# Performance work log

Hardware: AMD Instinct MI355X
Metric: run time of the kernel (lower is better)

Reference implementation:

```python
import jax, jax.numpy as jnp
import numpy as np

HIDDEN = 512
TEXT_DIM = 768
NUM_HEADS = 8
NUM_GROUPS = 32
GN_EPS = 1e-5
COS_EPS = 1e-6


def setup_inputs() -> dict:
    key = jax.random.key(0)
    ks = jax.random.split(key, 9)
    s = 0.02
    return {
        "x": jax.random.normal(ks[0], (16, HIDDEN, 64, 64), jnp.float32),
        "text_emb": jax.random.normal(ks[1], (16, 77, TEXT_DIM), jnp.float32),
        "gn_weight": jnp.ones((HIDDEN,), jnp.float32),
        "gn_bias": jnp.zeros((HIDDEN,), jnp.float32),
        "Wq": jax.random.normal(ks[2], (HIDDEN, HIDDEN), jnp.float32) * s,
        "Wk": jax.random.normal(ks[3], (HIDDEN, TEXT_DIM), jnp.float32) * s,
        "Wv": jax.random.normal(ks[4], (HIDDEN, TEXT_DIM), jnp.float32) * s,
        "Wo": jax.random.normal(ks[5], (HIDDEN, HIDDEN), jnp.float32) * s,
        "bo": jnp.zeros((HIDDEN,), jnp.float32),
    }


def reference(x, text_emb, gn_weight, gn_bias, Wq, Wk, Wv, Wo, bo):
    B, C, H, W = x.shape
    N_img = H * W
    nh, hd = NUM_HEADS, C // NUM_HEADS

    # GroupNorm(32, C): normalize over (channels-in-group, H, W)
    xg = x.reshape(B, NUM_GROUPS, -1)
    mu = xg.mean(axis=-1, keepdims=True)
    var = jnp.mean(jnp.square(xg - mu), axis=-1, keepdims=True)
    xn = ((xg - mu) * jax.lax.rsqrt(var + GN_EPS)).reshape(B, C, H, W)
    xn = xn * gn_weight[None, :, None, None] + gn_bias[None, :, None, None]

    x_flat = xn.reshape(B, C, N_img).transpose(0, 2, 1)  # [B, N_img, C]

    q = jnp.einsum('bnc,dc->bnd', x_flat, Wq)            # [B, N_img, C]
    k = jnp.einsum('btc,dc->btd', text_emb, Wk)          # [B, N_text, C]
    v = jnp.einsum('btc,dc->btd', text_emb, Wv)

    # split heads -> [B, nh, N, hd]
    q = q.reshape(B, N_img, nh, hd).transpose(0, 2, 1, 3)
    k = k.reshape(B, -1, nh, hd).transpose(0, 2, 1, 3)
    v = v.reshape(B, -1, nh, hd).transpose(0, 2, 1, 3)

    # cosine-sim attention: L2-normalize q and k, scale = 1.0
    q = q / (jnp.linalg.norm(q, axis=-1, keepdims=True) + COS_EPS)
    k = k / (jnp.linalg.norm(k, axis=-1, keepdims=True) + COS_EPS)

    scores = jnp.einsum('bhqd,bhkd->bhqk', q, k)         # [B, nh, N_img, N_text]
    attn = jax.nn.softmax(scores, axis=-1)
    out = jnp.einsum('bhqk,bhkd->bhqd', attn, v)         # [B, nh, N_img, hd]

    out = out.transpose(0, 2, 1, 3).reshape(B, N_img, C)
    out = jnp.einsum('bnc,dc->bnd', out, Wo) + bo
    out = out.transpose(0, 2, 1).reshape(B, C, H, W)
    return x + out
```

## Files before the change

### kernel.cpp

```cpp
#include <hip/hip_runtime.h>
#include <math.h>


typedef unsigned short u16;
typedef __attribute__((ext_vector_type(8))) __bf16 bf16x8;
typedef __attribute__((ext_vector_type(4))) float f32x4;

typedef __attribute__((address_space(1))) unsigned int as1_u32;
typedef __attribute__((address_space(3))) unsigned int as3_u32;

__device__ __forceinline__ float b2f(u16 u) {
  union { unsigned int i; float f; } c; c.i = ((unsigned int)u) << 16; return c.f;
}
__device__ __forceinline__ u16 f2b(float f) {
  union { float f; unsigned int i; } c; c.f = f;
  unsigned int i = c.i + 0x7fffu + ((c.i >> 16) & 1u);
  return (u16)(i >> 16);
}

__device__ __forceinline__ void g2lds16(const void* g, void* l) {
  __builtin_amdgcn_global_load_lds((const as1_u32*)g, (as3_u32*)l, 16, 0, 0);
}

__global__ void k_cast(const float* __restrict__ in, u16* __restrict__ out, int n) {
  int i = blockIdx.x * 256 + threadIdx.x;
  int st = gridDim.x * 256;
  for (; i < n; i += st) out[i] = f2b(in[i]);
}

__global__ __launch_bounds__(256) void k_gnstats(const float* __restrict__ x,
                                                 float* __restrict__ stats) {
  int bg = blockIdx.x;
  const float4* p = (const float4*)(x + (size_t)bg * 65536);
  float s = 0.f, ss = 0.f;
  for (int i = threadIdx.x; i < 16384; i += 256) {
    float4 v = p[i];
    s  += v.x + v.y + v.z + v.w;
    ss += v.x*v.x + v.y*v.y + v.z*v.z + v.w*v.w;
  }
  for (int o = 1; o < 64; o <<= 1) { s += __shfl_xor(s, o, 64); ss += __shfl_xor(ss, o, 64); }
  __shared__ float as_[4], bs_[4];
  int w = threadIdx.x >> 6;
  if ((threadIdx.x & 63) == 0) { as_[w] = s; bs_[w] = ss; }
  __syncthreads();
  if (threadIdx.x == 0) {
    s  = as_[0] + as_[1] + as_[2] + as_[3];
    ss = bs_[0] + bs_[1] + bs_[2] + bs_[3];
    float mu  = s * (1.f / 65536.f);
    float var = ss * (1.f / 65536.f) - mu * mu;
    stats[2*bg]   = mu;
    stats[2*bg+1] = rsqrtf(var + 1e-5f);
  }
}

__global__ __launch_bounds__(256) void k_gnapply(
    const float* __restrict__ x, const float* __restrict__ stats,
    const float* __restrict__ gw, const float* __restrict__ gb,
    u16* __restrict__ xn) {
  __shared__ float tile[64][65];
  const int b = blockIdx.z, c0 = blockIdx.y << 6, hw0 = blockIdx.x << 6;
  const int t = threadIdx.x;
  const int tl16 = t & 15;
#pragma unroll
  for (int i = 0; i < 4; ++i) {
    const int cl = (i << 4) + (t >> 4);
    const int c = c0 + cl;
    const int sg = (b << 5) + (c >> 4);
    const float mu = stats[2*sg], rs = stats[2*sg+1];
    const float wgt = gw[c] * rs, bs = gb[c] - mu * wgt;
    const float4 v = *(const float4*)(x + (((size_t)b << 9) + c) * 4096 + hw0 + (tl16 << 2));
    tile[cl][(tl16 << 2) + 0] = v.x * wgt + bs;
    tile[cl][(tl16 << 2) + 1] = v.y * wgt + bs;
    tile[cl][(tl16 << 2) + 2] = v.z * wgt + bs;
    tile[cl][(tl16 << 2) + 3] = v.w * wgt + bs;
  }
  __syncthreads();
#pragma unroll
  for (int i = 0; i < 4; ++i) {
    const int hl = (i << 4) + (t >> 4);
    const int c4 = tl16 << 2;
    ushort4 o;
    o.x = f2b(tile[c4 + 0][hl]);
    o.y = f2b(tile[c4 + 1][hl]);
    o.z = f2b(tile[c4 + 2][hl]);
    o.w = f2b(tile[c4 + 3][hl]);
    *(ushort4*)(xn + ((size_t)((b << 12) + hw0 + hl)) * 512 + c0 + c4) = o;
  }
}

template <int MODE>
__global__ __launch_bounds__(256) void k_gemm(
    const u16* __restrict__ A, const u16* __restrict__ BT,
    int M, int N, int K,
    float* __restrict__ outf, u16* __restrict__ outb,
    const float* __restrict__ xres, const float* __restrict__ bias) {
  __shared__ u16 Al[2][128 * 64];
  __shared__ u16 Bl[2][128 * 64];
  const int tid = threadIdx.x;
  const int l = tid & 63, w = tid >> 6;

  const int nwg = gridDim.x * gridDim.y;
  int lin = blockIdx.y * gridDim.x + blockIdx.x;
  lin = (lin & 7) * (nwg >> 3) + (lin >> 3);
  const int m0 = (lin / gridDim.x) << 7, n0 = (lin % gridDim.x) << 7;

  const int wm = (w >> 1) << 6, wn = (w & 1) << 6;
  const int lr = l & 15, lg = l >> 4;

  f32x4 acc[4][4];
#pragma unroll
  for (int i = 0; i < 4; ++i)
#pragma unroll
    for (int j = 0; j < 4; ++j) acc[i][j] = {0.f, 0.f, 0.f, 0.f};

  const int rl = l >> 3, slot = l & 7;
  const int c8 = (slot ^ rl) << 3;
  int arow[4], brow[4];
#pragma unroll
  for (int j = 0; j < 4; ++j) {
    const int r_local = (w << 5) + (j << 3) + rl;
    arow[j] = min(m0 + r_local, M - 1);
    brow[j] = n0 + r_local;
  }

  const int ksteps = K >> 6;

#pragma unroll
  for (int j = 0; j < 4; ++j)
    g2lds16(A + (size_t)arow[j] * K + c8, Al[0] + (((w << 5) + (j << 3)) << 6));
#pragma unroll
  for (int j = 0; j < 4; ++j)
    g2lds16(BT + (size_t)brow[j] * K + c8, Bl[0] + (((w << 5) + (j << 3)) << 6));
  __syncthreads();

  for (int ks = 0; ks < ksteps; ++ks) {
    const int cur = ks & 1, nxt = cur ^ 1;
    if (ks + 1 < ksteps) {
      const int kb = ((ks + 1) << 6) + c8;
#pragma unroll
      for (int j = 0; j < 4; ++j)
        g2lds16(A + (size_t)arow[j] * K + kb, Al[nxt] + (((w << 5) + (j << 3)) << 6));
#pragma unroll
      for (int j = 0; j < 4; ++j)
        g2lds16(BT + (size_t)brow[j] * K + kb, Bl[nxt] + (((w << 5) + (j << 3)) << 6));
    }
    bf16x8 bfr[4][2];
#pragma unroll
    for (int j = 0; j < 4; ++j) {
      const int br = wn + j * 16 + lr;
      bfr[j][0] = *(const bf16x8*)(Bl[cur] + (br << 6) + (((lg    ) ^ (br & 7)) << 3));
      bfr[j][1] = *(const bf16x8*)(Bl[cur] + (br << 6) + (((lg + 4) ^ (br & 7)) << 3));
    }
#pragma unroll
    for (int i = 0; i < 4; ++i) {
      const int ar = wm + i * 16 + lr;
      const bf16x8 a0 = *(const bf16x8*)(Al[cur] + (ar << 6) + (((lg    ) ^ (ar & 7)) << 3));
      const bf16x8 a1 = *(const bf16x8*)(Al[cur] + (ar << 6) + (((lg + 4) ^ (ar & 7)) << 3));
#pragma unroll
      for (int j = 0; j < 4; ++j) {
        acc[i][j] = __builtin_amdgcn_mfma_f32_16x16x32_bf16(a0, bfr[j][0], acc[i][j], 0, 0, 0);
        acc[i][j] = __builtin_amdgcn_mfma_f32_16x16x32_bf16(a1, bfr[j][1], acc[i][j], 0, 0, 0);
      }
    }
    __syncthreads();
  }

  const int lg4 = lg << 2;
  if (MODE == 3) {
#pragma unroll
    for (int i = 0; i < 4; ++i) {
#pragma unroll
      for (int r = 0; r < 4; ++r) {
        float ss = 0.f;
#pragma unroll
        for (int j = 0; j < 4; ++j) { const float v = acc[i][j][r]; ss += v * v; }
        ss += __shfl_xor(ss, 1, 64); ss += __shfl_xor(ss, 2, 64);
        ss += __shfl_xor(ss, 4, 64); ss += __shfl_xor(ss, 8, 64);
        const float sc = 1.f / (sqrtf(ss) + 1e-6f);
        const int row = m0 + wm + i * 16 + lg4 + r;
#pragma unroll
        for (int j = 0; j < 4; ++j)
          outb[(size_t)row * N + n0 + wn + j * 16 + lr] = f2b(acc[i][j][r] * sc);
      }
    }
    return;
  }
#pragma unroll
  for (int i = 0; i < 4; ++i) {
#pragma unroll
    for (int j = 0; j < 4; ++j) {
#pragma unroll
      for (int r = 0; r < 4; ++r) {
        const int row = m0 + wm + i * 16 + lg4 + r;
        const int col = n0 + wn + j * 16 + lr;
        const float v = acc[i][j][r];
        if (MODE == 0) {
          if (row < M) outf[(size_t)row * N + col] = v;
        } else if (MODE == 1) {
          outb[(size_t)row * N + col] = f2b(v);
        } else {
          const int bb = col >> 12, hw = col & 4095;
          const size_t o = (((size_t)bb << 9) + row) * 4096 + hw;
          outf[o] = xres[o] + bias[row] + v;
        }
      }
    }
  }
}

__global__ __launch_bounds__(64) void k_kvnorm(const float* __restrict__ kv,
                                               u16* __restrict__ kn,
                                               u16* __restrict__ vn) {
  const int row = blockIdx.x;
  const int h = blockIdx.y;
  const int d = threadIdx.x;
  const int b = row / 77, t = row - b * 77;
  const float kx = kv[(size_t)row * 1024 + h * 64 + d];
  float ss = kx * kx;
  for (int o = 1; o < 64; o <<= 1) ss += __shfl_xor(ss, o, 64);
  const float sc = 1.f / (sqrtf(ss) + 1e-6f);
  const size_t ob = (((size_t)(b * 8 + h)) * 77 + t) * 64 + d;
  kn[ob] = f2b(kx * sc);
  vn[ob] = f2b(kv[(size_t)row * 1024 + 512 + h * 64 + d]);
}

__global__ __launch_bounds__(256) void k_attn2(
    const u16* __restrict__ q, const u16* __restrict__ kn,
    const u16* __restrict__ vn, u16* __restrict__ out) {
  __shared__ u16 Kl[96 * 72];
  __shared__ u16 Vt[64 * 104];
  __shared__ u16 Pl[64 * 104];
  const int qt = blockIdx.x, h = blockIdx.y, b = blockIdx.z;
  const size_t kvb = ((size_t)(b * 8 + h)) * (77 * 64);
  const int tid = threadIdx.x;
  for (int u = tid; u < 768; u += 256) {
    const int row = u >> 3, c8v = (u & 7) << 3;
    uint4 v = make_uint4(0, 0, 0, 0);
    if (row < 77) v = *(const uint4*)(kn + kvb + row * 64 + c8v);
    *(uint4*)(Kl + row * 72 + c8v) = v;
  }
  for (int u = tid; u < 768; u += 256) {
    const int row = u >> 3, c8v = (u & 7) << 3;
    uint4 v = make_uint4(0, 0, 0, 0);
    if (row < 77) v = *(const uint4*)(vn + kvb + row * 64 + c8v);
    const u16* pv = (const u16*)&v;
#pragma unroll
    for (int j = 0; j < 8; ++j) Vt[(c8v + j) * 104 + row] = pv[j];
  }
  __syncthreads();
  const int l = tid & 63, w = tid >> 6;
  const int lr = l & 15, lg = l >> 4;

  const int qrow = (b << 12) + (qt << 6) + (w << 4) + lr;
  bf16x8 af0 = *(const bf16x8*)(q + (size_t)qrow * 512 + h * 64 + lg * 8);
  bf16x8 af1 = *(const bf16x8*)(q + (size_t)qrow * 512 + h * 64 + 32 + lg * 8);
  f32x4 s[6];
#pragma unroll
  for (int nt = 0; nt < 6; ++nt) {
    s[nt] = {0.f, 0.f, 0.f, 0.f};
    bf16x8 bk0 = *(const bf16x8*)(Kl + (nt * 16 + lr) * 72 + lg * 8);
    bf16x8 bk1 = *(const bf16x8*)(Kl + (nt * 16 + lr) * 72 + 32 + lg * 8);
    s[nt] = __builtin_amdgcn_mfma_f32_16x16x32_bf16(af0, bk0, s[nt], 0, 0, 0);
    s[nt] = __builtin_amdgcn_mfma_f32_16x16x32_bf16(af1, bk1, s[nt], 0, 0, 0);
  }
#pragma unroll
  for (int r = 0; r < 4; ++r) {
    if (lr >= 13) s[4][r] = -1e30f;
    s[5][r] = -1e30f;
  }
#pragma unroll
  for (int r = 0; r < 4; ++r) {
    float m = s[0][r];
#pragma unroll
    for (int nt = 1; nt < 6; ++nt) m = fmaxf(m, s[nt][r]);
    m = fmaxf(m, __shfl_xor(m, 1, 64)); m = fmaxf(m, __shfl_xor(m, 2, 64));
    m = fmaxf(m, __shfl_xor(m, 4, 64)); m = fmaxf(m, __shfl_xor(m, 8, 64));
    float sum = 0.f;
#pragma unroll
    for (int nt = 0; nt < 6; ++nt) { s[nt][r] = __expf(s[nt][r] - m); sum += s[nt][r]; }
    sum += __shfl_xor(sum, 1, 64); sum += __shfl_xor(sum, 2, 64);
    sum += __shfl_xor(sum, 4, 64); sum += __shfl_xor(sum, 8, 64);
    const float inv = 1.f / sum;
    const int qlocal = (w << 4) + (lg << 2) + r;
#pragma unroll
    for (int nt = 0; nt < 6; ++nt)
      Pl[qlocal * 104 + nt * 16 + lr] = f2b(s[nt][r] * inv);
  }
  __syncthreads();

  bf16x8 pa0 = *(const bf16x8*)(Pl + ((w << 4) + lr) * 104 + lg * 8);
  bf16x8 pa1 = *(const bf16x8*)(Pl + ((w << 4) + lr) * 104 + 32 + lg * 8);
  bf16x8 pa2 = *(const bf16x8*)(Pl + ((w << 4) + lr) * 104 + 64 + lg * 8);
  f32x4 o[4];
#pragma unroll
  for (int nt = 0; nt < 4; ++nt) {
    o[nt] = {0.f, 0.f, 0.f, 0.f};
    bf16x8 bv0 = *(const bf16x8*)(Vt + (nt * 16 + lr) * 104 + lg * 8);
    bf16x8 bv1 = *(const bf16x8*)(Vt + (nt * 16 + lr) * 104 + 32 + lg * 8);
    bf16x8 bv2 = *(const bf16x8*)(Vt + (nt * 16 + lr) * 104 + 64 + lg * 8);
    o[nt] = __builtin_amdgcn_mfma_f32_16x16x32_bf16(pa0, bv0, o[nt], 0, 0, 0);
    o[nt] = __builtin_amdgcn_mfma_f32_16x16x32_bf16(pa1, bv1, o[nt], 0, 0, 0);
    o[nt] = __builtin_amdgcn_mfma_f32_16x16x32_bf16(pa2, bv2, o[nt], 0, 0, 0);
  }
#pragma unroll
  for (int r = 0; r < 4; ++r) {
    const int n = (b << 12) + (qt << 6) + (w << 4) + (lg << 2) + r;
#pragma unroll
    for (int nt = 0; nt < 4; ++nt)
      out[(size_t)n * 512 + h * 64 + nt * 16 + lr] = f2b(o[nt][r]);
  }
}

extern "C" void kernel_launch(void* const* d_in, const int* in_sizes, int n_in,
                              void* d_out, int out_size, void* d_ws, size_t ws_size,
                              hipStream_t stream) {
  (void)in_sizes; (void)n_in; (void)out_size; (void)ws_size;
  const float* x    = (const float*)d_in[0];
  const float* text = (const float*)d_in[1];
  const float* gnw  = (const float*)d_in[2];
  const float* gnb  = (const float*)d_in[3];
  const float* Wq   = (const float*)d_in[4];
  const float* Wk   = (const float*)d_in[5];
  const float* Wv   = (const float*)d_in[6];
  const float* Wo   = (const float*)d_in[7];
  const float* bo   = (const float*)d_in[8];
  float* out = (float*)d_out;

  char* ws = (char*)d_ws;
  size_t off = 0;
  auto alloc = [&](size_t bytes) -> void* {
    void* p = ws + off; off += (bytes + 255) & ~(size_t)255; return p;
  };
  float* stats = (float*)alloc(512 * 2 * 4);
  u16* wq_b    = (u16*)alloc((size_t)512 * 512 * 2);
  u16* wkv_b   = (u16*)alloc((size_t)1024 * 768 * 2);
  u16* wo_b    = (u16*)alloc((size_t)512 * 512 * 2);
  u16* text_b  = (u16*)alloc((size_t)1232 * 768 * 2);
  float* kv_f  = (float*)alloc((size_t)1232 * 1024 * 4);
  u16* kn      = (u16*)alloc((size_t)16 * 8 * 77 * 64 * 2);
  u16* vn      = (u16*)alloc((size_t)16 * 8 * 77 * 64 * 2);
  u16* xn      = (u16*)alloc((size_t)65536 * 512 * 2);
  u16* qb      = (u16*)alloc((size_t)65536 * 512 * 2);

  k_cast<<<dim3(256), 256, 0, stream>>>(Wq, wq_b, 512 * 512);
  k_cast<<<dim3(256), 256, 0, stream>>>(Wk, wkv_b, 512 * 768);
  k_cast<<<dim3(256), 256, 0, stream>>>(Wv, wkv_b + 512 * 768, 512 * 768);
  k_cast<<<dim3(256), 256, 0, stream>>>(Wo, wo_b, 512 * 512);
  k_cast<<<dim3(512), 256, 0, stream>>>(text, text_b, 1232 * 768);

  k_gnstats<<<dim3(512), 256, 0, stream>>>(x, stats);
  k_gnapply<<<dim3(64, 8, 16), 256, 0, stream>>>(x, stats, gnw, gnb, xn);

  k_gemm<0><<<dim3(8, 10), 256, 0, stream>>>(text_b, wkv_b, 1232, 1024, 768,
                                             kv_f, nullptr, nullptr, nullptr);
  k_kvnorm<<<dim3(1232, 8), 64, 0, stream>>>(kv_f, kn, vn);

  k_gemm<3><<<dim3(4, 512), 256, 0, stream>>>(xn, wq_b, 65536, 512, 512,
                                              nullptr, qb, nullptr, nullptr);

  k_attn2<<<dim3(64, 8, 16), 256, 0, stream>>>(qb, kn, vn, xn);

  k_gemm<2><<<dim3(512, 4), 256, 0, stream>>>(wo_b, xn, 512, 65536, 512,
                                              out, nullptr, x, bo);
}
```

Baseline: 322.3 us.

## Fuse GroupNorm apply into Q projection GEMM and merge cast kernels

Result: faster. 307.6 us (-4.6%).

```diff
diff --git a/kernel.cpp b/kernel.cpp
--- a/kernel.cpp
+++ b/kernel.cpp
@@ -22,10 +22,17 @@
   __builtin_amdgcn_global_load_lds((const as1_u32*)g, (as3_u32*)l, 16, 0, 0);
 }
 
-__global__ void k_cast(const float* __restrict__ in, u16* __restrict__ out, int n) {
-  int i = blockIdx.x * 256 + threadIdx.x;
-  int st = gridDim.x * 256;
-  for (; i < n; i += st) out[i] = f2b(in[i]);
+__global__ void k_castall(const float* __restrict__ Wq, const float* __restrict__ Wk,
+                          const float* __restrict__ Wv, const float* __restrict__ Wo,
+                          const float* __restrict__ text,
+                          u16* __restrict__ wq_b, u16* __restrict__ wkv_b,
+                          u16* __restrict__ wo_b, u16* __restrict__ text_b) {
+  const int i = blockIdx.x * 256 + threadIdx.x, st = gridDim.x * 256;
+  for (int j = i; j < 262144; j += st) wq_b[j] = f2b(Wq[j]);
+  for (int j = i; j < 393216; j += st) wkv_b[j] = f2b(Wk[j]);
+  for (int j = i; j < 393216; j += st) wkv_b[393216 + j] = f2b(Wv[j]);
+  for (int j = i; j < 262144; j += st) wo_b[j] = f2b(Wo[j]);
+  for (int j = i; j < 946176; j += st) text_b[j] = f2b(text[j]);
 }
 
 __global__ __launch_bounds__(256) void k_gnstats(const float* __restrict__ x,
@@ -53,38 +60,107 @@
   }
 }
 
-__global__ __launch_bounds__(256) void k_gnapply(
+__global__ __launch_bounds__(256) void k_qproj(
     const float* __restrict__ x, const float* __restrict__ stats,
     const float* __restrict__ gw, const float* __restrict__ gb,
-    u16* __restrict__ xn) {
-  __shared__ float tile[64][65];
-  const int b = blockIdx.z, c0 = blockIdx.y << 6, hw0 = blockIdx.x << 6;
-  const int t = threadIdx.x;
-  const int tl16 = t & 15;
+    const u16* __restrict__ Wqb, u16* __restrict__ qb) {
+  __shared__ u16 Al[128 * 64];
+  __shared__ u16 Bl[128 * 64];
+  __shared__ float cw[512], cb[512];
+  const int tid = threadIdx.x;
+  const int o = blockIdx.x;
+  const int mi = ((o >> 5) << 3) + (o & 7);
+  const int ni = (o >> 3) & 3;
+  const int m0 = mi << 7, n0 = ni << 7;
+  const int b = m0 >> 12, hw0 = m0 & 4095;
+
+  for (int c = tid; c < 512; c += 256) {
+    const int g = (b << 5) + (c >> 4);
+    const float mu = stats[2*g], rs = stats[2*g+1];
+    const float wg = gw[c] * rs;
+    cw[c] = wg; cb[c] = gb[c] - mu * wg;
+  }
+
+  const int l = tid & 63, w = tid >> 6;
+  const int wm = (w >> 1) << 6, wn = (w & 1) << 6;
+  const int lr = l & 15, lg = l >> 4;
+
+  f32x4 acc[4][4];
+#pragma unroll
+  for (int i = 0; i < 4; ++i)
+#pragma unroll
+    for (int j = 0; j < 4; ++j) acc[i][j] = {0.f, 0.f, 0.f, 0.f};
+
+  const int rl = l >> 3, slot = l & 7;
+  const int c8 = (slot ^ rl) << 3;
+  int brow[4];
+#pragma unroll
+  for (int j = 0; j < 4; ++j) brow[j] = n0 + (w << 5) + (j << 3) + rl;
+
+  const int tokl = tid & 127;
+  const int chg = tid >> 7;
+  const float* xb = x + (((size_t)b) << 9) * 4096;
+  __syncthreads();
+
+  for (int ks = 0; ks < 8; ++ks) {
+#pragma unroll
+    for (int j = 0; j < 4; ++j)
+      g2lds16(Wqb + (size_t)brow[j] * 512 + (ks << 6) + c8,
+              Bl + (((w << 5) + (j << 3)) << 6));
+#pragma unroll
+    for (int jj = 0; jj < 8; ++jj) {
+      const int ch4 = (((chg << 3) + jj) << 2);
+      const int c = (ks << 6) + ch4;
+      const float v0 = xb[(size_t)(c + 0) * 4096 + hw0 + tokl];
+      const float v1 = xb[(size_t)(c + 1) * 4096 + hw0 + tokl];
+      const float v2 = xb[(size_t)(c + 2) * 4096 + hw0 + tokl];
+      const float v3 = xb[(size_t)(c + 3) * 4096 + hw0 + tokl];
+      ushort4 pk;
+      pk.x = f2b(v0 * cw[c + 0] + cb[c + 0]);
+      pk.y = f2b(v1 * cw[c + 1] + cb[c + 1]);
+      pk.z = f2b(v2 * cw[c + 2] + cb[c + 2]);
+      pk.w = f2b(v3 * cw[c + 3] + cb[c + 3]);
+      const int sl = (((ch4 >> 3) ^ (tokl & 7)) << 3) + (ch4 & 7);
+      *(ushort4*)(Al + (tokl << 6) + sl) = pk;
+    }
+    __syncthreads();
+    bf16x8 bfr[4][2];
+#pragma unroll
+    for (int j = 0; j < 4; ++j) {
+      const int br = wn + j * 16 + lr;
+      bfr[j][0] = *(const bf16x8*)(Bl + (br << 6) + (((lg    ) ^ (br & 7)) << 3));
+      bfr[j][1] = *(const bf16x8*)(Bl + (br << 6) + (((lg + 4) ^ (br & 7)) << 3));
+    }
+#pragma unroll
+    for (int i = 0; i < 4; ++i) {
+      const int ar = wm + i * 16 + lr;
+      const bf16x8 a0 = *(const bf16x8*)(Al + (ar << 6) + (((lg    ) ^ (ar & 7)) << 3));
+      const bf16x8 a1 = *(const bf16x8*)(Al + (ar << 6) + (((lg + 4) ^ (ar & 7)) << 3));
+#pragma unroll
+      for (int j = 0; j < 4; ++j) {
+        acc[i][j] = __builtin_amdgcn_mfma_f32_16x16x32_bf16(a0, bfr[j][0], acc[i][j], 0, 0, 0);
+        acc[i][j] = __builtin_amdgcn_mfma_f32_16x16x32_bf16(a1, bfr[j][1], acc[i][j], 0, 0, 0);
+      }
+    }
+    __syncthreads();
+  }
+
+  const int lg4 = lg << 2;
 #pragma unroll
   for (int i = 0; i < 4; ++i) {
-    const int cl = (i << 4) + (t >> 4);
-    const int c = c0 + cl;
-    const int sg = (b << 5) + (c >> 4);
-    const float mu = stats[2*sg], rs = stats[2*sg+1];
-    const float wgt = gw[c] * rs, bs = gb[c] - mu * wgt;
-    const float4 v = *(const float4*)(x + (((size_t)b << 9) + c) * 4096 + hw0 + (tl16 << 2));
-    tile[cl][(tl16 << 2) + 0] = v.x * wgt + bs;
-    tile[cl][(tl16 << 2) + 1] = v.y * wgt + bs;
-    tile[cl][(tl16 << 2) + 2] = v.z * wgt + bs;
-    tile[cl][(tl16 << 2) + 3] = v.w * wgt + bs;
-  }
-  __syncthreads();
-#pragma unroll
-  for (int i = 0; i < 4; ++i) {
-    const int hl = (i << 4) + (t >> 4);
-    const int c4 = tl16 << 2;
-    ushort4 o;
-    o.x = f2b(tile[c4 + 0][hl]);
-    o.y = f2b(tile[c4 + 1][hl]);
-    o.z = f2b(tile[c4 + 2][hl]);
-    o.w = f2b(tile[c4 + 3][hl]);
-    *(ushort4*)(xn + ((size_t)((b << 12) + hw0 + hl)) * 512 + c0 + c4) = o;
+#pragma unroll
+    for (int r = 0; r < 4; ++r) {
+      float ss = 0.f;
+#pragma unroll
+      for (int j = 0; j < 4; ++j) { const float v = acc[i][j][r]; ss += v * v; }
+      ss += __shfl_xor(ss, 1, 64); ss += __shfl_xor(ss, 2, 64);
+      ss += __shfl_xor(ss, 4, 64); ss += __shfl_xor(ss, 8, 64);
+      const float sc = 1.f / (sqrtf(ss) + 1e-6f);
+      const int row = m0 + wm + i * 16 + lg4 + r;
+#pragma unroll
+      for (int j = 0; j < 4; ++j)
+        qb[(size_t)row * 512 + n0 + wn + j * 16 + lr] = f2b(acc[i][j][r] * sc);
+    }
   }
 }
 
@@ -124,7 +200,6 @@
   }
 
   const int ksteps = K >> 6;
-
 #pragma unroll
   for (int j = 0; j < 4; ++j)
     g2lds16(A + (size_t)arow[j] * K + c8, Al[0] + (((w << 5) + (j << 3)) << 6));
@@ -166,25 +241,6 @@
   }
 
   const int lg4 = lg << 2;
-  if (MODE == 3) {
-#pragma unroll
-    for (int i = 0; i < 4; ++i) {
-#pragma unroll
-      for (int r = 0; r < 4; ++r) {
-        float ss = 0.f;
-#pragma unroll
-        for (int j = 0; j < 4; ++j) { const float v = acc[i][j][r]; ss += v * v; }
-        ss += __shfl_xor(ss, 1, 64); ss += __shfl_xor(ss, 2, 64);
-        ss += __shfl_xor(ss, 4, 64); ss += __shfl_xor(ss, 8, 64);
-        const float sc = 1.f / (sqrtf(ss) + 1e-6f);
-        const int row = m0 + wm + i * 16 + lg4 + r;
-#pragma unroll
-        for (int j = 0; j < 4; ++j)
-          outb[(size_t)row * N + n0 + wn + j * 16 + lr] = f2b(acc[i][j][r] * sc);
-      }
-    }
-    return;
-  }
 #pragma unroll
   for (int i = 0; i < 4; ++i) {
 #pragma unroll
@@ -196,8 +252,6 @@
         const float v = acc[i][j][r];
         if (MODE == 0) {
           if (row < M) outf[(size_t)row * N + col] = v;
-        } else if (MODE == 1) {
-          outb[(size_t)row * N + col] = f2b(v);
         } else {
           const int bb = col >> 12, hw = col & 4095;
           const size_t o = (((size_t)bb << 9) + row) * 4096 + hw;
@@ -339,27 +393,22 @@
   float* kv_f  = (float*)alloc((size_t)1232 * 1024 * 4);
   u16* kn      = (u16*)alloc((size_t)16 * 8 * 77 * 64 * 2);
   u16* vn      = (u16*)alloc((size_t)16 * 8 * 77 * 64 * 2);
-  u16* xn      = (u16*)alloc((size_t)65536 * 512 * 2);
+  u16* ao      = (u16*)alloc((size_t)65536 * 512 * 2);
   u16* qb      = (u16*)alloc((size_t)65536 * 512 * 2);
 
-  k_cast<<<dim3(256), 256, 0, stream>>>(Wq, wq_b, 512 * 512);
-  k_cast<<<dim3(256), 256, 0, stream>>>(Wk, wkv_b, 512 * 768);
-  k_cast<<<dim3(256), 256, 0, stream>>>(Wv, wkv_b + 512 * 768, 512 * 768);
-  k_cast<<<dim3(256), 256, 0, stream>>>(Wo, wo_b, 512 * 512);
-  k_cast<<<dim3(512), 256, 0, stream>>>(text, text_b, 1232 * 768);
+  k_castall<<<dim3(512), 256, 0, stream>>>(Wq, Wk, Wv, Wo, text,
+                                           wq_b, wkv_b, wo_b, text_b);
 
   k_gnstats<<<dim3(512), 256, 0, stream>>>(x, stats);
-  k_gnapply<<<dim3(64, 8, 16), 256, 0, stream>>>(x, stats, gnw, gnb, xn);
 
   k_gemm<0><<<dim3(8, 10), 256, 0, stream>>>(text_b, wkv_b, 1232, 1024, 768,
                                              kv_f, nullptr, nullptr, nullptr);
   k_kvnorm<<<dim3(1232, 8), 64, 0, stream>>>(kv_f, kn, vn);
 
-  k_gemm<3><<<dim3(4, 512), 256, 0, stream>>>(xn, wq_b, 65536, 512, 512,
-                                              nullptr, qb, nullptr, nullptr);
-
-  k_attn2<<<dim3(64, 8, 16), 256, 0, stream>>>(qb, kn, vn, xn);
-
-  k_gemm<2><<<dim3(512, 4), 256, 0, stream>>>(wo_b, xn, 512, 65536, 512,
+  k_qproj<<<dim3(2048), 256, 0, stream>>>(x, stats, gnw, gnb, wq_b, qb);
+
+  k_attn2<<<dim3(64, 8, 16), 256, 0, stream>>>(qb, kn, vn, ao);
+
+  k_gemm<2><<<dim3(512, 4), 256, 0, stream>>>(wo_b, ao, 512, 65536, 512,
                                               out, nullptr, x, bo);
 }
```
